# Performance work log

Hardware: AMD Instinct MI355X
Metric: run time of the kernel (lower is better)

Reference implementation:

```python
import jax, jax.numpy as jnp
import numpy as np

N_HEADS = 32
N_KV_HEADS = 8
HEAD_DIM = 128
ROPE_BASE = 10000.0
NEG_INF = -1e9


def rope(x, base=ROPE_BASE, offset=0):
    # x: [B, H, L, d]; 'traditional' RoPE with the module's rotation formula.
    d = x.shape[-1]
    t = jnp.arange(x.shape[2], dtype=jnp.float32) + offset
    freqs = base ** (-jnp.arange(0, d, 2, dtype=jnp.float32) / d)  # [d/2]
    ang = t[:, None] * freqs[None, :]                              # [L, d/2]
    cos, sin = jnp.cos(ang), jnp.sin(ang)
    x1, x2 = x[..., 0::2], x[..., 1::2]
    out = jnp.stack([x1 * cos + x2 * sin, x1 * sin - x2 * cos], axis=-1)
    return out.reshape(x.shape)


def setup_inputs() -> dict:
    key = jax.random.key(0)
    ks = jax.random.split(key, 5)
    B, L, D = 2, 2048, 4096
    x = jax.random.normal(ks[0], (B, L, D), dtype=jnp.float32)
    wq = jax.random.normal(ks[1], (D, N_HEADS * HEAD_DIM), dtype=jnp.float32) * 0.02
    wk = jax.random.normal(ks[2], (D, N_KV_HEADS * HEAD_DIM), dtype=jnp.float32) * 0.02
    wv = jax.random.normal(ks[3], (D, N_KV_HEADS * HEAD_DIM), dtype=jnp.float32) * 0.02
    wo = jax.random.normal(ks[4], (N_HEADS * HEAD_DIM, D), dtype=jnp.float32) * 0.02
    # causal additive mask [L, L]
    mask = jnp.where(jnp.tril(jnp.ones((L, L), dtype=bool)), 0.0, NEG_INF).astype(jnp.float32)
    return {"x": x, "mask": mask, "wq": wq, "wk": wk, "wv": wv, "wo": wo}


def reference(x, mask, wq, wk, wv, wo):
    B, L, D = x.shape
    scale = HEAD_DIM ** -0.5
    q = (x @ wq).reshape(B, L, N_HEADS, HEAD_DIM).transpose(0, 2, 1, 3)     # [B,H,L,d]
    k = (x @ wk).reshape(B, L, N_KV_HEADS, HEAD_DIM).transpose(0, 2, 1, 3)  # [B,Hk,L,d]
    v = (x @ wv).reshape(B, L, N_KV_HEADS, HEAD_DIM).transpose(0, 2, 1, 3)
    rep = N_HEADS // N_KV_HEADS
    k = jnp.repeat(k, rep, axis=1)  # [B,H,L,d]  (physical GQA repeat, as in source)
    v = jnp.repeat(v, rep, axis=1)
    q = rope(q)
    k = rope(k)
    scores = jnp.einsum("bhqd,bhkd->bhqk", q * scale, k) + mask  # [B,H,L,L]
    probs = jax.nn.softmax(scores.astype(jnp.float32), axis=-1).astype(scores.dtype)
    out = jnp.einsum("bhqk,bhkd->bhqd", probs, v)
    out = out.transpose(0, 2, 1, 3).reshape(B, L, N_HEADS * HEAD_DIM)
    return out @ wo, (k, v)
```

## Files before the change

kernel.cpp:

```cpp
#include <hip/hip_runtime.h>

typedef unsigned short u16;
typedef unsigned int u32;
typedef float f32x4 __attribute__((ext_vector_type(4)));
typedef __bf16 bf16x8 __attribute__((ext_vector_type(8)));

#define DEV __device__ __forceinline__

DEV u16 f2b(float f) {
    union { float f; u32 u; } v; v.f = f;
    u32 r = v.u + 0x7fffu + ((v.u >> 16) & 1u);
    return (u16)(r >> 16);
}
DEV float b2f(u16 b) {
    union { u32 u; float f; } v; v.u = ((u32)b) << 16;
    return v.f;
}

DEV void gload16(const void* g, void* l) {
    __builtin_amdgcn_global_load_lds((const __attribute__((address_space(1))) void*)g,
                                     (__attribute__((address_space(3))) void*)l, 16, 0, 0);
}

DEV f32x4 mfma16(bf16x8 a, bf16x8 b, f32x4 c) {
    return __builtin_amdgcn_mfma_f32_16x16x32_bf16(a, b, c, 0, 0, 0);
}

__global__ __launch_bounds__(256) void convx_kernel(const float* __restrict__ in,
                                                    u16* __restrict__ out) {
    size_t i = ((size_t)blockIdx.x * 256 + threadIdx.x) * 4;
    float4 v = *(const float4*)(in + i);
    ushort4 o; o.x = f2b(v.x); o.y = f2b(v.y); o.z = f2b(v.z); o.w = f2b(v.w);
    *(ushort4*)(out + i) = o;
}

__global__ __launch_bounds__(256) void tconv_kernel(const float* __restrict__ in,
                                                    u16* __restrict__ out, int K, int N) {
    __shared__ float tile[64][65];
    int t = threadIdx.x;
    int n0 = blockIdx.x * 64, k0 = blockIdx.y * 64;
    int r = t >> 4, c4 = (t & 15) * 4;
#pragma unroll
    for (int i = 0; i < 4; ++i) {
        float4 v = *(const float4*)(in + (size_t)(k0 + i * 16 + r) * N + n0 + c4);
        tile[i * 16 + r][c4 + 0] = v.x; tile[i * 16 + r][c4 + 1] = v.y;
        tile[i * 16 + r][c4 + 2] = v.z; tile[i * 16 + r][c4 + 3] = v.w;
    }
    __syncthreads();
#pragma unroll
    for (int i = 0; i < 4; ++i) {
        int nn = i * 16 + r;
        ushort4 o;
        o.x = f2b(tile[c4 + 0][nn]); o.y = f2b(tile[c4 + 1][nn]);
        o.z = f2b(tile[c4 + 2][nn]); o.w = f2b(tile[c4 + 3][nn]);
        *(ushort4*)(out + (size_t)(n0 + nn) * K + k0 + c4) = o;
    }
}

__global__ __launch_bounds__(512, 1) void gemm192_kernel(const u16* __restrict__ A,
                                                         const u16* __restrict__ Bt,
                                                         u16* __restrict__ Cb,
                                                         int N, int K, int gy) {
    __shared__ __align__(16) u16 Asb[2][2][128 * 64];
    __shared__ __align__(16) u16 Bsb[2][192 * 64];
    int t = threadIdx.x;
    int lane = t & 63, w = t >> 6;
    int wrM = w >> 2, wcN = w & 3;
    int lr = lane & 15, hi = lane >> 4;
    int wg = blockIdx.x;
    int swz = (wg & 7) * ((int)gridDim.x >> 3) + (wg >> 3);
    int bx = swz / gy, by = swz % gy;
    int m0 = by * 256, n0 = bx * 192;
    int nk = K >> 6;

    auto stageA = [&](int X) {
        const u16* src = A + (size_t)m0 * K + X * 64;
        char* dst = (char*)&Asb[X & 1][0][0];
#pragma unroll
        for (int it = 0; it < 4; ++it) {
            int c = it * 512 + t;
            int row = c >> 3;
            int col8 = ((c & 7) ^ (row & 7)) << 3;
            gload16(src + (size_t)row * K + col8, dst + (it * 512 + (t & ~63)) * 16);
        }
    };
    auto stageB = [&](int X) {
        const u16* src = Bt + (size_t)n0 * K + X * 64;
        char* dst = (char*)&Bsb[X & 1][0];
#pragma unroll
        for (int it = 0; it < 3; ++it) {
            int c = it * 512 + t;
            int row = c >> 3;
            int col8 = ((c & 7) ^ (row & 7)) << 3;
            gload16(src + (size_t)row * K + col8, dst + (it * 512 + (t & ~63)) * 16);
        }
    };

    stageA(0); stageB(0); stageA(1); stageB(1);
    asm volatile("s_waitcnt vmcnt(7)" ::: "memory");
    __builtin_amdgcn_s_barrier();

    f32x4 acc[8][3] = {};
    for (int kt = 0; kt < nk; ++kt) {
        __builtin_amdgcn_sched_barrier(0);
        int p = kt & 1;
        const char* Ah = (const char*)&Asb[p][wrM][0];
        const char* Bh = (const char*)&Bsb[p][0];
        bool s1 = (kt + 1 < nk), s2 = (kt + 2 < nk);
        bf16x8 a[8][2], bb[2][2], bc[2];

#pragma unroll
        for (int mf = 0; mf < 4; ++mf)
#pragma unroll
            for (int ks = 0; ks < 2; ++ks) {
                int row = mf * 16 + lr;
                int byt = (row * 128 + ks * 64 + hi * 16) ^ ((row & 7) << 4);
                a[mf][ks] = *(const bf16x8*)(Ah + byt);
            }
#pragma unroll
        for (int nf = 0; nf < 2; ++nf)
#pragma unroll
            for (int ks = 0; ks < 2; ++ks) {
                int row = wcN * 48 + nf * 16 + lr;
                int byt = (row * 128 + ks * 64 + hi * 16) ^ ((row & 7) << 4);
                bb[nf][ks] = *(const bf16x8*)(Bh + byt);
            }
        __builtin_amdgcn_s_barrier();
        __builtin_amdgcn_s_setprio(1);
#pragma unroll
        for (int mf = 0; mf < 4; ++mf)
#pragma unroll
            for (int nf = 0; nf < 2; ++nf)
#pragma unroll
                for (int ks = 0; ks < 2; ++ks)
                    acc[mf][nf] = mfma16(a[mf][ks], bb[nf][ks], acc[mf][nf]);
        __builtin_amdgcn_s_setprio(0);
        __builtin_amdgcn_s_barrier();

#pragma unroll
        for (int mf = 4; mf < 8; ++mf)
#pragma unroll
            for (int ks = 0; ks < 2; ++ks) {
                int row = mf * 16 + lr;
                int byt = (row * 128 + ks * 64 + hi * 16) ^ ((row & 7) << 4);
                a[mf][ks] = *(const bf16x8*)(Ah + byt);
            }
        __builtin_amdgcn_s_barrier();
        __builtin_amdgcn_s_setprio(1);
#pragma unroll
        for (int mf = 4; mf < 8; ++mf)
#pragma unroll
            for (int nf = 0; nf < 2; ++nf)
#pragma unroll
                for (int ks = 0; ks < 2; ++ks)
                    acc[mf][nf] = mfma16(a[mf][ks], bb[nf][ks], acc[mf][nf]);
        __builtin_amdgcn_s_setprio(0);
        __builtin_amdgcn_s_barrier();

#pragma unroll
        for (int ks = 0; ks < 2; ++ks) {
            int row = wcN * 48 + 32 + lr;
            int byt = (row * 128 + ks * 64 + hi * 16) ^ ((row & 7) << 4);
            bc[ks] = *(const bf16x8*)(Bh + byt);
        }
        if (s2) stageA(kt + 2);
        __builtin_amdgcn_s_barrier();
        __builtin_amdgcn_s_setprio(1);
#pragma unroll
        for (int mf = 4; mf < 8; ++mf)
#pragma unroll
            for (int ks = 0; ks < 2; ++ks)
                acc[mf][2] = mfma16(a[mf][ks], bc[ks], acc[mf][2]);
        __builtin_amdgcn_s_setprio(0);
        __builtin_amdgcn_s_barrier();

        if (s2) stageB(kt + 2);
        __builtin_amdgcn_s_barrier();
        __builtin_amdgcn_s_setprio(1);
#pragma unroll
        for (int mf = 0; mf < 4; ++mf)
#pragma unroll
            for (int ks = 0; ks < 2; ++ks)
                acc[mf][2] = mfma16(a[mf][ks], bc[ks], acc[mf][2]);
        __builtin_amdgcn_s_setprio(0);
        if (s1) {
            if (s2) asm volatile("s_waitcnt vmcnt(7)" ::: "memory");
            else    asm volatile("s_waitcnt vmcnt(0)" ::: "memory");
        }
        __builtin_amdgcn_s_barrier();
    }

#pragma unroll
    for (int mf = 0; mf < 8; ++mf)
#pragma unroll
        for (int nf = 0; nf < 3; ++nf)
#pragma unroll
            for (int r = 0; r < 4; ++r) {
                int m = m0 + wrM * 128 + mf * 16 + hi * 4 + r;
                int n = n0 + wcN * 48 + nf * 16 + lr;
                Cb[(size_t)m * N + n] = f2b(acc[mf][nf][r]);
            }
}

template <bool F32OUT>
__global__ __launch_bounds__(512, 1) void gemm256_kernel(const u16* __restrict__ A,
                                                         const u16* __restrict__ Bt,
                                                         u16* __restrict__ Cb,
                                                         float* __restrict__ Cf,
                                                         int M, int N, int K, int gy) {
    __shared__ __align__(16) u16 Asb[2][2][128 * 64];
    __shared__ __align__(16) u16 Bsb[2][2][128 * 64];
    (void)M;
    int t = threadIdx.x;
    int lane = t & 63, w = t >> 6;
    int wrM = w >> 2, wcN = w & 3;
    int lr = lane & 15, hi = lane >> 4;
    int wg = blockIdx.x;
    int swz = (wg & 7) * ((int)gridDim.x >> 3) + (wg >> 3);
    int bx = swz / gy, by = swz % gy;
    int m0 = by * 256, n0 = bx * 256;
    int nk = K >> 6;

    auto stageA = [&](int X, int h) {
        const u16* src = A + (size_t)(m0 + h * 128) * K + X * 64;
        char* dst = (char*)&Asb[X & 1][h][0];
#pragma unroll
        for (int it = 0; it < 2; ++it) {
            int c = it * 512 + t;
            int row = c >> 3;
            int col8 = ((c & 7) ^ (row & 7)) << 3;
            gload16(src + (size_t)row * K + col8, dst + (it * 512 + (t & ~63)) * 16);
        }
    };
    auto stageB = [&](int X, int h) {
        const u16* src = Bt + (size_t)(n0 + h * 128) * K + X * 64;
        char* dst = (char*)&Bsb[X & 1][h][0];
#pragma unroll
        for (int it = 0; it < 2; ++it) {
            int c = it * 512 + t;
            int row = c >> 3;
            int col8 = ((c & 7) ^ (row & 7)) << 3;
            gload16(src + (size_t)row * K + col8, dst + (it * 512 + (t & ~63)) * 16);
        }
    };

    stageA(0, 0); stageA(0, 1); stageB(0, 0); stageB(0, 1);
    stageA(1, 0); stageA(1, 1); stageB(1, 0);
    asm volatile("s_waitcnt vmcnt(6)" ::: "memory");
    __builtin_amdgcn_s_barrier();

    f32x4 acc[8][4] = {};
    for (int kt = 0; kt < nk; ++kt) {
        __builtin_amdgcn_sched_barrier(0);
        int p = kt & 1;
        const char* Ah = (const char*)&Asb[p][wrM][0];
        const char* Bh = (const char*)&Bsb[p][wcN >> 1][0];
        bool s1 = (kt + 1 < nk), s2 = (kt + 2 < nk);
        bf16x8 a[8][2], bb[2][2];

#pragma unroll
        for (int mf = 0; mf < 4; ++mf)
#pragma unroll
            for (int ks = 0; ks < 2; ++ks) {
                int row = mf * 16 + lr;
                int byt = (row * 128 + ks * 64 + hi * 16) ^ ((row & 7) << 4);
                a[mf][ks] = *(const bf16x8*)(Ah + byt);
            }
#pragma unroll
        for (int nf = 0; nf < 2; ++nf)
#pragma unroll
            for (int ks = 0; ks < 2; ++ks) {
                int row = (wcN & 1) * 64 + nf * 16 + lr;
                int byt = (row * 128 + ks * 64 + hi * 16) ^ ((row & 7) << 4);
                bb[nf][ks] = *(const bf16x8*)(Bh + byt);
            }
        if (s1) stageB(kt + 1, 1);
        __builtin_amdgcn_s_barrier();
        __builtin_amdgcn_s_setprio(1);
#pragma unroll
        for (int mf = 0; mf < 4; ++mf)
#pragma unroll
            for (int nf = 0; nf < 2; ++nf)
#pragma unroll
                for (int ks = 0; ks < 2; ++ks)
                    acc[mf][nf] = mfma16(a[mf][ks], bb[nf][ks], acc[mf][nf]);
        __builtin_amdgcn_s_setprio(0);
        __builtin_amdgcn_s_barrier();

#pragma unroll
        for (int mf = 4; mf < 8; ++mf)
#pragma unroll
            for (int ks = 0; ks < 2; ++ks) {
                int row = mf * 16 + lr;
                int byt = (row * 128 + ks * 64 + hi * 16) ^ ((row & 7) << 4);
                a[mf][ks] = *(const bf16x8*)(Ah + byt);
            }
        __builtin_amdgcn_s_barrier();
        __builtin_amdgcn_s_setprio(1);
#pragma unroll
        for (int mf = 4; mf < 8; ++mf)
#pragma unroll
            for (int nf = 0; nf < 2; ++nf)
#pragma unroll
                for (int ks = 0; ks < 2; ++ks)
                    acc[mf][nf] = mfma16(a[mf][ks], bb[nf][ks], acc[mf][nf]);
        __builtin_amdgcn_s_setprio(0);
        __builtin_amdgcn_s_barrier();

#pragma unroll
        for (int nf = 0; nf < 2; ++nf)
#pragma unroll
            for (int ks = 0; ks < 2; ++ks) {
                int row = (wcN & 1) * 64 + (nf + 2) * 16 + lr;
                int byt = (row * 128 + ks * 64 + hi * 16) ^ ((row & 7) << 4);
                bb[nf][ks] = *(const bf16x8*)(Bh + byt);
            }
        if (s2) { stageA(kt + 2, 0); stageA(kt + 2, 1); }
        __builtin_amdgcn_s_barrier();
        __builtin_amdgcn_s_setprio(1);
#pragma unroll
        for (int mf = 4; mf < 8; ++mf)
#pragma unroll
            for (int nf = 0; nf < 2; ++nf)
#pragma unroll
                for (int ks = 0; ks < 2; ++ks)
                    acc[mf][nf + 2] = mfma16(a[mf][ks], bb[nf][ks], acc[mf][nf + 2]);
        __builtin_amdgcn_s_setprio(0);
        __builtin_amdgcn_s_barrier();

        if (s2) stageB(kt + 2, 0);
        __builtin_amdgcn_s_barrier();
        __builtin_amdgcn_s_setprio(1);
#pragma unroll
        for (int mf = 0; mf < 4; ++mf)
#pragma unroll
            for (int nf = 0; nf < 2; ++nf)
#pragma unroll
                for (int ks = 0; ks < 2; ++ks)
                    acc[mf][nf + 2] = mfma16(a[mf][ks], bb[nf][ks], acc[mf][nf + 2]);
        __builtin_amdgcn_s_setprio(0);
        if (s1) {
            if (s2) asm volatile("s_waitcnt vmcnt(6)" ::: "memory");
            else    asm volatile("s_waitcnt vmcnt(0)" ::: "memory");
        }
        __builtin_amdgcn_s_barrier();
    }

#pragma unroll
    for (int mf = 0; mf < 8; ++mf)
#pragma unroll
        for (int nf = 0; nf < 4; ++nf)
#pragma unroll
            for (int r = 0; r < 4; ++r) {
                int m = m0 + wrM * 128 + mf * 16 + hi * 4 + r;
                int n = n0 + wcN * 64 + nf * 16 + lr;
                if (F32OUT) Cf[(size_t)m * N + n] = acc[mf][nf][r];
                else        Cb[(size_t)m * N + n] = f2b(acc[mf][nf][r]);
            }
}

__global__ __launch_bounds__(256) void rope_kernel(u16* __restrict__ qkv,
                                                   float* __restrict__ outk) {
    int row = blockIdx.y;
    int p = blockIdx.x * 256 + threadIdx.x;
    int b = row >> 11, l = row & 2047;
    float freq = exp2f((float)(p & 63) * -0.2076205059304601f);
    float sv, cv; sincosf((float)l * freq, &sv, &cv);
    if (p < 2048) {
        int h = p >> 6, i = p & 63;
        size_t idx = (size_t)row * 6144 + h * 128 + 2 * i;
        u32 pr = *(const u32*)(qkv + idx);
        float x1 = b2f((u16)(pr & 0xffff)), x2 = b2f((u16)(pr >> 16));
        float o1 = x1 * cv + x2 * sv, o2 = x1 * sv - x2 * cv;
        *(u32*)(qkv + idx) = (u32)f2b(o1) | ((u32)f2b(o2) << 16);
    } else {
        int kvh = (p >> 6) - 32, i = p & 63;
        size_t idx = (size_t)row * 6144 + 4096 + kvh * 128 + 2 * i;
        u32 pr = *(const u32*)(qkv + idx);
        float x1 = b2f((u16)(pr & 0xffff)), x2 = b2f((u16)(pr >> 16));
        float o1 = x1 * cv + x2 * sv, o2 = x1 * sv - x2 * cv;
        *(u32*)(qkv + idx) = (u32)f2b(o1) | ((u32)f2b(o2) << 16);
#pragma unroll
        for (int r = 0; r < 4; ++r) {
            float2 o; o.x = o1; o.y = o2;
            *(float2*)(outk + ((size_t)((b * 32 + kvh * 4 + r) * 2048) + l) * 128 + 2 * i) = o;
        }
    }
}

__global__ __launch_bounds__(256) void vtrans_kernel(const u16* __restrict__ qkv,
                                                     u16* __restrict__ vt,
                                                     float* __restrict__ outv) {
    __shared__ u16 tile[64][65];
    int t = threadIdx.x;
    int l0 = blockIdx.x * 64, d0 = blockIdx.y * 64;
    int z = blockIdx.z, b = z >> 3, kvh = z & 7;
    int r = t >> 4, c4 = (t & 15) * 4;
#pragma unroll
    for (int i = 0; i < 4; ++i) {
        int l = l0 + i * 16 + r;
        ushort4 v = *(const ushort4*)(qkv + (size_t)(b * 2048 + l) * 6144 + 5120 + kvh * 128 + d0 + c4);
        tile[i * 16 + r][c4 + 0] = v.x; tile[i * 16 + r][c4 + 1] = v.y;
        tile[i * 16 + r][c4 + 2] = v.z; tile[i * 16 + r][c4 + 3] = v.w;
        float4 f; f.x = b2f(v.x); f.y = b2f(v.y); f.z = b2f(v.z); f.w = b2f(v.w);
#pragma unroll
        for (int rr = 0; rr < 4; ++rr)
            *(float4*)(outv + ((size_t)((b * 32 + kvh * 4 + rr) * 2048) + l) * 128 + d0 + c4) = f;
    }
    __syncthreads();
#pragma unroll
    for (int i = 0; i < 4; ++i) {
        int dn = i * 16 + r;
        ushort4 o;
        o.x = tile[c4 + 0][dn]; o.y = tile[c4 + 1][dn];
        o.z = tile[c4 + 2][dn]; o.w = tile[c4 + 3][dn];
        *(ushort4*)(vt + (size_t)((b * 8 + kvh) * 128 + d0 + dn) * 2048 + l0 + c4) = o;
    }
}

__global__ __launch_bounds__(256) void attn_kernel(const u16* __restrict__ qkv,
                                                   const u16* __restrict__ vt,
                                                   u16* __restrict__ ab) {
    __shared__ __align__(16) u16 Kbuf[2][64 * 128];
    __shared__ __align__(16) u16 Vbuf[2][128 * 64];
    __shared__ __align__(16) u16 Ps[4][16 * 64];
    int t = threadIdx.x, lane = t & 63, w = t >> 6;
    int lr = lane & 15, hi = lane >> 4;
    int h = blockIdx.y, b = blockIdx.z, kvh = h >> 2;

    const u16* kbase = qkv + (size_t)(b * 2048) * 6144 + 4096 + kvh * 128;
    const u16* vtbase = vt + (size_t)((b * 8 + kvh) * 128) * 2048;

    auto stageKV = [&](int k0, int buf) {
#pragma unroll
        for (int i = 0; i < 4; ++i) {
            int c = i * 256 + t;
            int row = c >> 4;
            int col8 = ((c & 15) ^ (row & 7)) << 3;
            gload16(kbase + (size_t)(k0 + row) * 6144 + col8,
                    (char*)Kbuf[buf] + (i * 256 + (t & ~63)) * 16);
        }
#pragma unroll
        for (int i = 0; i < 4; ++i) {
            int c = i * 256 + t;
            int row = c >> 3;
            int col8 = ((c & 7) ^ (row & 7)) << 3;
            gload16(vtbase + (size_t)row * 2048 + k0 + col8,
                    (char*)Vbuf[buf] + (i * 256 + (t & ~63)) * 16);
        }
    };

    auto process = [&](int qblk) {
        int q0 = qblk * 64;
        int qr = w * 16 + lr;
        bf16x8 qf[4];
#pragma unroll
        for (int kki = 0; kki < 4; ++kki)
            qf[kki] = *(const bf16x8*)(qkv + (size_t)(b * 2048 + q0 + qr) * 6144 + h * 128 +
                                       kki * 32 + 8 * hi);
        f32x4 acc[8] = {};
        float mrun[4], lrun[4];
#pragma unroll
        for (int r = 0; r < 4; ++r) { mrun[r] = -1e30f; lrun[r] = 0.f; }

        int nt = qblk + 1;
        stageKV(0, 0);
        __syncthreads();
        int cur = 0;
        for (int kt = 0; kt < nt; ++kt) {
            if (kt + 1 < nt) stageKV((kt + 1) * 64, cur ^ 1);
            __builtin_amdgcn_sched_barrier(0);

            const u16* Ks = Kbuf[cur];
            const u16* Vs = Vbuf[cur];
            f32x4 s[4] = {};
            __builtin_amdgcn_s_setprio(1);
#pragma unroll
            for (int kki = 0; kki < 4; ++kki) {
                bf16x8 kf[4];
#pragma unroll
                for (int fc = 0; fc < 4; ++fc) {
                    int kvr = fc * 16 + lr;
                    int byt = (kvr * 256 + (kki * 32 + 8 * hi) * 2) ^ ((kvr & 7) << 4);
                    kf[fc] = *(const bf16x8*)((const char*)Ks + byt);
                }
#pragma unroll
                for (int fc = 0; fc < 4; ++fc) s[fc] = mfma16(qf[kki], kf[fc], s[fc]);
            }
            __builtin_amdgcn_s_setprio(0);
            const float SC = 0.08838834764831845f;
            int diag = (kt == nt - 1);
#pragma unroll
            for (int fc = 0; fc < 4; ++fc)
#pragma unroll
                for (int r = 0; r < 4; ++r) {
                    float v = s[fc][r] * SC;
                    if (diag && (fc * 16 + lr) > (w * 16 + hi * 4 + r)) v = -1e30f;
                    s[fc][r] = v;
                }
            float fr[4];
#pragma unroll
            for (int r = 0; r < 4; ++r) {
                float v = fmaxf(fmaxf(s[0][r], s[1][r]), fmaxf(s[2][r], s[3][r]));
                v = fmaxf(v, __shfl_xor(v, 1)); v = fmaxf(v, __shfl_xor(v, 2));
                v = fmaxf(v, __shfl_xor(v, 4)); v = fmaxf(v, __shfl_xor(v, 8));
                float mn = fmaxf(mrun[r], v);
                fr[r] = __expf(mrun[r] - mn);
                mrun[r] = mn;
            }
#pragma unroll
            for (int fc = 0; fc < 4; ++fc)
#pragma unroll
                for (int r = 0; r < 4; ++r) s[fc][r] = __expf(s[fc][r] - mrun[r]);
#pragma unroll
            for (int r = 0; r < 4; ++r) {
                float v = s[0][r] + s[1][r] + s[2][r] + s[3][r];
                v += __shfl_xor(v, 1); v += __shfl_xor(v, 2);
                v += __shfl_xor(v, 4); v += __shfl_xor(v, 8);
                lrun[r] = lrun[r] * fr[r] + v;
            }
#pragma unroll
            for (int dhf = 0; dhf < 8; ++dhf)
#pragma unroll
                for (int r = 0; r < 4; ++r) acc[dhf][r] *= fr[r];
            u16* Pw = Ps[w];
#pragma unroll
            for (int fc = 0; fc < 4; ++fc)
#pragma unroll
                for (int r = 0; r < 4; ++r) {
                    int prow = hi * 4 + r, pcol = fc * 16 + lr;
                    int byt = (prow * 128 + pcol * 2) ^ ((prow & 7) << 4);
                    *(u16*)((char*)Pw + byt) = f2b(s[fc][r]);
                }
            asm volatile("s_waitcnt lgkmcnt(0)" ::: "memory");
            __builtin_amdgcn_s_setprio(1);
#pragma unroll
            for (int kk2 = 0; kk2 < 2; ++kk2) {
                int bytp = (lr * 128 + (kk2 * 32 + 8 * hi) * 2) ^ ((lr & 7) << 4);
                bf16x8 pf = *(const bf16x8*)((const char*)Pw + bytp);
#pragma unroll
                for (int dhf = 0; dhf < 8; ++dhf) {
                    int dh = dhf * 16 + lr;
                    int bytv = (dh * 128 + (kk2 * 32 + 8 * hi) * 2) ^ ((dh & 7) << 4);
                    bf16x8 vf = *(const bf16x8*)((const char*)Vs + bytv);
                    acc[dhf] = mfma16(pf, vf, acc[dhf]);
                }
            }
            __builtin_amdgcn_s_setprio(0);
            __syncthreads();
            cur ^= 1;
        }
#pragma unroll
        for (int dhf = 0; dhf < 8; ++dhf)
#pragma unroll
            for (int r = 0; r < 4; ++r) {
                int qrow = q0 + w * 16 + hi * 4 + r;
                int dh = dhf * 16 + lr;
                ab[(size_t)(b * 2048 + qrow) * 4096 + h * 128 + dh] = f2b(acc[dhf][r] / lrun[r]);
            }
    };

    process(31 - blockIdx.x);
    __syncthreads();
    process(blockIdx.x);
}

extern "C" void kernel_launch(void* const* d_in, const int* in_sizes, int n_in,
                              void* d_out, int out_size, void* d_ws, size_t ws_size,
                              hipStream_t stream) {
    (void)in_sizes; (void)n_in; (void)out_size; (void)ws_size;
    const float* x  = (const float*)d_in[0];
    const float* wq = (const float*)d_in[2];
    const float* wk = (const float*)d_in[3];
    const float* wv = (const float*)d_in[4];
    const float* wo = (const float*)d_in[5];

    char* ws = (char*)d_ws;
    u16* xb  = (u16*)(ws + 0);
    u16* fBt = (u16*)(ws + 33554432);
    u16* qkv = (u16*)(ws + 83886080);
    u16* vt  = (u16*)(ws + 134217728);
    u16* ab  = xb;
    u16* wob = fBt;

    float* out0 = (float*)d_out;
    float* outk = out0 + 16777216;
    float* outv = out0 + 33554432;

    convx_kernel<<<16384, 256, 0, stream>>>(x, xb);
    tconv_kernel<<<dim3(64, 64), 256, 0, stream>>>(wq, fBt, 4096, 4096);
    tconv_kernel<<<dim3(16, 64), 256, 0, stream>>>(wk, fBt + (size_t)4096 * 4096, 4096, 1024);
    tconv_kernel<<<dim3(16, 64), 256, 0, stream>>>(wv, fBt + (size_t)5120 * 4096, 4096, 1024);

    gemm192_kernel<<<512, 512, 0, stream>>>(xb, fBt, qkv, 6144, 4096, 16);

    tconv_kernel<<<dim3(64, 64), 256, 0, stream>>>(wo, wob, 4096, 4096);

    rope_kernel<<<dim3(10, 4096), 256, 0, stream>>>(qkv, outk);
    vtrans_kernel<<<dim3(32, 2, 16), 256, 0, stream>>>(qkv, vt, outv);

    attn_kernel<<<dim3(16, 32, 2), 256, 0, stream>>>(qkv, vt, ab);

    gemm256_kernel<true><<<256, 512, 0, stream>>>(ab, wob, nullptr, out0, 4096, 4096, 4096, 16);
}
```

Measured before the change: 650.8 us.

## Transpose attention MFMA operands so each lane owns one query row

The QK^T and PV MFMAs in the attention kernel now take their operands in swapped order, so the score and output tiles come out transposed and each lane holds a single query row. This makes the softmax row state scalar per lane. Row max and sum reductions drop from four xor-shuffles per row over four rows to two cross-group shuffles on one value. P is written to LDS as packed 8-byte stores, and the output is written as 8-byte vector stores using one reciprocal multiply instead of per-element divides. The GEMM kernels only receive a cosmetic inlining of the address computation.

```diff
diff --git a/kernel.cpp b/kernel.cpp
--- a/kernel.cpp
+++ b/kernel.cpp
@@ -3,6 +3,7 @@
 typedef unsigned short u16;
 typedef unsigned int u32;
 typedef float f32x4 __attribute__((ext_vector_type(4)));
+typedef u32 u32x2 __attribute__((ext_vector_type(2)));
 typedef __bf16 bf16x8 __attribute__((ext_vector_type(8)));
 
 #define DEV __device__ __forceinline__
@@ -114,16 +115,14 @@
 #pragma unroll
             for (int ks = 0; ks < 2; ++ks) {
                 int row = mf * 16 + lr;
-                int byt = (row * 128 + ks * 64 + hi * 16) ^ ((row & 7) << 4);
-                a[mf][ks] = *(const bf16x8*)(Ah + byt);
+                a[mf][ks] = *(const bf16x8*)(Ah + ((row * 128 + ks * 64 + hi * 16) ^ ((row & 7) << 4)));
             }
 #pragma unroll
         for (int nf = 0; nf < 2; ++nf)
 #pragma unroll
             for (int ks = 0; ks < 2; ++ks) {
                 int row = wcN * 48 + nf * 16 + lr;
-                int byt = (row * 128 + ks * 64 + hi * 16) ^ ((row & 7) << 4);
-                bb[nf][ks] = *(const bf16x8*)(Bh + byt);
+                bb[nf][ks] = *(const bf16x8*)(Bh + ((row * 128 + ks * 64 + hi * 16) ^ ((row & 7) << 4)));
             }
         __builtin_amdgcn_s_barrier();
         __builtin_amdgcn_s_setprio(1);
@@ -142,8 +141,7 @@
 #pragma unroll
             for (int ks = 0; ks < 2; ++ks) {
                 int row = mf * 16 + lr;
-                int byt = (row * 128 + ks * 64 + hi * 16) ^ ((row & 7) << 4);
-                a[mf][ks] = *(const bf16x8*)(Ah + byt);
+                a[mf][ks] = *(const bf16x8*)(Ah + ((row * 128 + ks * 64 + hi * 16) ^ ((row & 7) << 4)));
             }
         __builtin_amdgcn_s_barrier();
         __builtin_amdgcn_s_setprio(1);
@@ -160,8 +158,7 @@
 #pragma unroll
         for (int ks = 0; ks < 2; ++ks) {
             int row = wcN * 48 + 32 + lr;
-            int byt = (row * 128 + ks * 64 + hi * 16) ^ ((row & 7) << 4);
-            bc[ks] = *(const bf16x8*)(Bh + byt);
+            bc[ks] = *(const bf16x8*)(Bh + ((row * 128 + ks * 64 + hi * 16) ^ ((row & 7) << 4)));
         }
         if (s2) stageA(kt + 2);
         __builtin_amdgcn_s_barrier();
@@ -263,16 +260,14 @@
 #pragma unroll
             for (int ks = 0; ks < 2; ++ks) {
                 int row = mf * 16 + lr;
-                int byt = (row * 128 + ks * 64 + hi * 16) ^ ((row & 7) << 4);
-                a[mf][ks] = *(const bf16x8*)(Ah + byt);
+                a[mf][ks] = *(const bf16x8*)(Ah + ((row * 128 + ks * 64 + hi * 16) ^ ((row & 7) << 4)));
             }
 #pragma unroll
         for (int nf = 0; nf < 2; ++nf)
 #pragma unroll
             for (int ks = 0; ks < 2; ++ks) {
                 int row = (wcN & 1) * 64 + nf * 16 + lr;
-                int byt = (row * 128 + ks * 64 + hi * 16) ^ ((row & 7) << 4);
-                bb[nf][ks] = *(const bf16x8*)(Bh + byt);
+                bb[nf][ks] = *(const bf16x8*)(Bh + ((row * 128 + ks * 64 + hi * 16) ^ ((row & 7) << 4)));
             }
         if (s1) stageB(kt + 1, 1);
         __builtin_amdgcn_s_barrier();
@@ -292,8 +287,7 @@
 #pragma unroll
             for (int ks = 0; ks < 2; ++ks) {
                 int row = mf * 16 + lr;
-                int byt = (row * 128 + ks * 64 + hi * 16) ^ ((row & 7) << 4);
-                a[mf][ks] = *(const bf16x8*)(Ah + byt);
+                a[mf][ks] = *(const bf16x8*)(Ah + ((row * 128 + ks * 64 + hi * 16) ^ ((row & 7) << 4)));
             }
         __builtin_amdgcn_s_barrier();
         __builtin_amdgcn_s_setprio(1);
@@ -312,8 +306,7 @@
 #pragma unroll
             for (int ks = 0; ks < 2; ++ks) {
                 int row = (wcN & 1) * 64 + (nf + 2) * 16 + lr;
-                int byt = (row * 128 + ks * 64 + hi * 16) ^ ((row & 7) << 4);
-                bb[nf][ks] = *(const bf16x8*)(Bh + byt);
+                bb[nf][ks] = *(const bf16x8*)(Bh + ((row * 128 + ks * 64 + hi * 16) ^ ((row & 7) << 4)));
             }
         if (s2) { stageA(kt + 2, 0); stageA(kt + 2, 1); }
         __builtin_amdgcn_s_barrier();
@@ -459,9 +452,7 @@
             qf[kki] = *(const bf16x8*)(qkv + (size_t)(b * 2048 + q0 + qr) * 6144 + h * 128 +
                                        kki * 32 + 8 * hi);
         f32x4 acc[8] = {};
-        float mrun[4], lrun[4];
-#pragma unroll
-        for (int r = 0; r < 4; ++r) { mrun[r] = -1e30f; lrun[r] = 0.f; }
+        float mrun = -1e30f, lrun = 0.f;
 
         int nt = qblk + 1;
         stageKV(0, 0);
@@ -485,7 +476,7 @@
                     kf[fc] = *(const bf16x8*)((const char*)Ks + byt);
                 }
 #pragma unroll
-                for (int fc = 0; fc < 4; ++fc) s[fc] = mfma16(qf[kki], kf[fc], s[fc]);
+                for (int fc = 0; fc < 4; ++fc) s[fc] = mfma16(kf[fc], qf[kki], s[fc]);
             }
             __builtin_amdgcn_s_setprio(0);
             const float SC = 0.08838834764831845f;
@@ -495,69 +486,71 @@
 #pragma unroll
                 for (int r = 0; r < 4; ++r) {
                     float v = s[fc][r] * SC;
-                    if (diag && (fc * 16 + lr) > (w * 16 + hi * 4 + r)) v = -1e30f;
+                    if (diag && (fc * 16 + hi * 4 + r) > qr) v = -1e30f;
                     s[fc][r] = v;
                 }
-            float fr[4];
-#pragma unroll
-            for (int r = 0; r < 4; ++r) {
-                float v = fmaxf(fmaxf(s[0][r], s[1][r]), fmaxf(s[2][r], s[3][r]));
-                v = fmaxf(v, __shfl_xor(v, 1)); v = fmaxf(v, __shfl_xor(v, 2));
-                v = fmaxf(v, __shfl_xor(v, 4)); v = fmaxf(v, __shfl_xor(v, 8));
-                float mn = fmaxf(mrun[r], v);
-                fr[r] = __expf(mrun[r] - mn);
-                mrun[r] = mn;
-            }
+            float pm = s[0][0];
 #pragma unroll
             for (int fc = 0; fc < 4; ++fc)
 #pragma unroll
-                for (int r = 0; r < 4; ++r) s[fc][r] = __expf(s[fc][r] - mrun[r]);
-#pragma unroll
-            for (int r = 0; r < 4; ++r) {
-                float v = s[0][r] + s[1][r] + s[2][r] + s[3][r];
-                v += __shfl_xor(v, 1); v += __shfl_xor(v, 2);
-                v += __shfl_xor(v, 4); v += __shfl_xor(v, 8);
-                lrun[r] = lrun[r] * fr[r] + v;
-            }
+                for (int r = 0; r < 4; ++r) pm = fmaxf(pm, s[fc][r]);
+            pm = fmaxf(pm, __shfl_xor(pm, 16));
+            pm = fmaxf(pm, __shfl_xor(pm, 32));
+            float mn = fmaxf(mrun, pm);
+            float fr = __expf(mrun - mn);
+            mrun = mn;
+            float ls = 0.f;
+#pragma unroll
+            for (int fc = 0; fc < 4; ++fc)
+#pragma unroll
+                for (int r = 0; r < 4; ++r) {
+                    float e = __expf(s[fc][r] - mn);
+                    s[fc][r] = e;
+                    ls += e;
+                }
+            ls += __shfl_xor(ls, 16);
+            ls += __shfl_xor(ls, 32);
+            lrun = lrun * fr + ls;
 #pragma unroll
             for (int dhf = 0; dhf < 8; ++dhf)
 #pragma unroll
-                for (int r = 0; r < 4; ++r) acc[dhf][r] *= fr[r];
+                for (int r = 0; r < 4; ++r) acc[dhf][r] *= fr;
             u16* Pw = Ps[w];
 #pragma unroll
-            for (int fc = 0; fc < 4; ++fc)
-#pragma unroll
-                for (int r = 0; r < 4; ++r) {
-                    int prow = hi * 4 + r, pcol = fc * 16 + lr;
-                    int byt = (prow * 128 + pcol * 2) ^ ((prow & 7) << 4);
-                    *(u16*)((char*)Pw + byt) = f2b(s[fc][r]);
-                }
+            for (int fc = 0; fc < 4; ++fc) {
+                u32x2 pk;
+                pk.x = (u32)f2b(s[fc][0]) | ((u32)f2b(s[fc][1]) << 16);
+                pk.y = (u32)f2b(s[fc][2]) | ((u32)f2b(s[fc][3]) << 16);
+                int byt = (lr * 128 + fc * 32 + hi * 8) ^ ((lr & 7) << 4);
+                *(u32x2*)((char*)Pw + byt) = pk;
+            }
             asm volatile("s_waitcnt lgkmcnt(0)" ::: "memory");
             __builtin_amdgcn_s_setprio(1);
 #pragma unroll
             for (int kk2 = 0; kk2 < 2; ++kk2) {
-                int bytp = (lr * 128 + (kk2 * 32 + 8 * hi) * 2) ^ ((lr & 7) << 4);
+                int bytp = (lr * 128 + kk2 * 64 + hi * 16) ^ ((lr & 7) << 4);
                 bf16x8 pf = *(const bf16x8*)((const char*)Pw + bytp);
 #pragma unroll
                 for (int dhf = 0; dhf < 8; ++dhf) {
                     int dh = dhf * 16 + lr;
                     int bytv = (dh * 128 + (kk2 * 32 + 8 * hi) * 2) ^ ((dh & 7) << 4);
                     bf16x8 vf = *(const bf16x8*)((const char*)Vs + bytv);
-                    acc[dhf] = mfma16(pf, vf, acc[dhf]);
+                    acc[dhf] = mfma16(vf, pf, acc[dhf]);
                 }
             }
             __builtin_amdgcn_s_setprio(0);
             __syncthreads();
             cur ^= 1;
         }
-#pragma unroll
-        for (int dhf = 0; dhf < 8; ++dhf)
-#pragma unroll
-            for (int r = 0; r < 4; ++r) {
-                int qrow = q0 + w * 16 + hi * 4 + r;
-                int dh = dhf * 16 + lr;
-                ab[(size_t)(b * 2048 + qrow) * 4096 + h * 128 + dh] = f2b(acc[dhf][r] / lrun[r]);
-            }
+        float inv = 1.0f / lrun;
+        int qrow = q0 + qr;
+#pragma unroll
+        for (int dhf = 0; dhf < 8; ++dhf) {
+            ushort4 o;
+            o.x = f2b(acc[dhf][0] * inv); o.y = f2b(acc[dhf][1] * inv);
+            o.z = f2b(acc[dhf][2] * inv); o.w = f2b(acc[dhf][3] * inv);
+            *(ushort4*)(ab + (size_t)(b * 2048 + qrow) * 4096 + h * 128 + dhf * 16 + hi * 4) = o;
+        }
     };
 
     process(31 - blockIdx.x);
```

Result: faster. 616.5 us (-5.3%).
